# Optimization experiments

Hardware: AMD Instinct MI355X
Metric: run time of the kernel (lower is better)

## Reference

```python
import jax, jax.numpy as jnp
import numpy as np

B, T, N, CIN = 16, 34, 1000, 32
DC, OC, E, DIL = 32, 64, 16000, 2


def _dilated_conv(xt, w, b, d):
    # xt: [B, C, N, T], w: [O, C, 1, 2] -> [B, O, N, T-d]
    Tt = xt.shape[-1]
    y = (jnp.einsum('bcnt,oc->bont', xt[..., :Tt - d], w[:, :, 0, 0])
         + jnp.einsum('bcnt,oc->bont', xt[..., d:], w[:, :, 0, 1]))
    return y + b[None, :, None, None]


def setup_inputs() -> dict:
    key = jax.random.key(0)
    ks = jax.random.split(key, 12)
    return {
        'x': jax.random.normal(ks[0], (B, T, N, CIN), jnp.float32),
        'edge_index': jax.random.randint(ks[1], (2, E), 0, N, jnp.int32),
        'edge_weight': jax.random.uniform(ks[2], (E,), jnp.float32),
        'w_gate1': jax.random.normal(ks[3], (DC, CIN, 1, 2), jnp.float32) * 0.1,
        'b_gate1': jax.random.normal(ks[4], (DC,), jnp.float32) * 0.1,
        'w_gate2': jax.random.normal(ks[5], (DC, CIN, 1, 2), jnp.float32) * 0.1,
        'b_gate2': jax.random.normal(ks[6], (DC,), jnp.float32) * 0.1,
        'w_gcn': jax.random.normal(ks[7], (CIN, DC), jnp.float32) * 0.1,
        'b_gcn': jax.random.normal(ks[8], (CIN,), jnp.float32) * 0.1,
        'w_out': jax.random.normal(ks[9], (OC, CIN, 1, 1), jnp.float32) * 0.1,
        'b_out': jax.random.normal(ks[10], (OC,), jnp.float32) * 0.1,
    }


def reference(x, edge_index, edge_weight, w_gate1, b_gate1, w_gate2, b_gate2,
              w_gcn, b_gcn, w_out, b_out):
    # [B,T,N,C] -> [B,C,N,T]  (torch transpose(-3,-1))
    xt = jnp.transpose(x, (0, 3, 2, 1))
    g1 = jnp.tanh(_dilated_conv(xt, w_gate1, b_gate1, DIL))
    g2 = jax.nn.sigmoid(_dilated_conv(xt, w_gate2, b_gate2, DIL))
    out1 = g1 * g2                      # [B, DC, N, T']
    Tp = out1.shape[-1]
    gated = jnp.transpose(out1, (0, 3, 2, 1))        # [B, T', N, DC]
    out2 = gated.reshape(B * Tp, N, DC)              # G graphs, shared adjacency

    # --- GCNConv (PyG defaults: add self-loops w=1, symmetric normalization) ---
    src, dst = edge_index[0], edge_index[1]
    loop = jnp.arange(N, dtype=edge_index.dtype)
    src_a = jnp.concatenate([src, loop])
    dst_a = jnp.concatenate([dst, loop])
    w_a = jnp.concatenate([edge_weight, jnp.ones((N,), edge_weight.dtype)])
    deg = jax.ops.segment_sum(w_a, dst_a, num_segments=N)
    dis = jnp.where(deg > 0, jax.lax.rsqrt(jnp.where(deg > 0, deg, 1.0)), 0.0)
    norm = dis[src_a] * w_a * dis[dst_a]
    # All G graphs share the adjacency -> build it once densely (N x N is tiny)
    A = jnp.zeros((N, N), out2.dtype).at[dst_a, src_a].add(norm)
    xw = jnp.einsum('gnd,cd->gnc', out2, w_gcn)      # linear: x @ W^T
    gcn = jnp.einsum('ij,gjc->gic', A, xw) + b_gcn   # propagate + bias
    gcn = gcn.reshape(B, Tp, N, CIN)
    # dropout: deterministic (eval) identity

    # 1x1 output conv (applied in NCHW, equivalent to per-channel linear)
    y = jnp.einsum('btnc,oc->btno', gcn, w_out[:, :, 0, 0]) + b_out
    return (out1, y)
```

## Files before the change

### kernel.cpp

```cpp
#include <hip/hip_runtime.h>
#include <math.h>

#define Bq 16
#define Tq 34
#define Nq 1000
#define Cq 32
#define OCq 64
#define Eq 16000
#define TPq 32
#define Gq (Bq*TPq)

typedef _Float16 f16;
typedef f16  f16x8 __attribute__((ext_vector_type(8)));
typedef float f32x4 __attribute__((ext_vector_type(4)));

__device__ __forceinline__ float fast_tanh(float x) {
    float xc = fminf(fmaxf(x, -15.f), 15.f);
    float u  = __expf(2.f * xc);
    return 1.f - 2.f * __builtin_amdgcn_rcpf(u + 1.f);
}
__device__ __forceinline__ float fast_sigmoid(float x) {
    float xc = fminf(fmaxf(x, -30.f), 30.f);
    return __builtin_amdgcn_rcpf(1.f + __expf(-xc));
}
__device__ __forceinline__ unsigned bf16_bits(float f) {
    unsigned u = __float_as_uint(f);
    return (u + 0x7fffu + ((u >> 16) & 1u)) >> 16;
}
__device__ __forceinline__ unsigned pack_bf16x2(float lo, float hi) {
    return bf16_bits(lo) | (bf16_bits(hi) << 16);
}

__global__ __launch_bounds__(640) void k_prep(
    const float* __restrict__ wg1, const float* __restrict__ wg2,
    const float* __restrict__ wgcn, f16* __restrict__ fragbuf)
{
    const int tid = threadIdx.x;
    if (tid < 512) {
        const int fid  = tid >> 6;
        const int lane = tid & 63;
        const int gate  = fid >> 2;
        const int otile = (fid >> 1) & 1;
        const int ks    = fid & 1;
        const float* w = gate ? wg2 : wg1;
        const int o = otile*16 + (lane & 15);
        f16* dst = fragbuf + (size_t)fid*512 + lane*8;
        #pragma unroll
        for (int j = 0; j < 8; j++) {
            const int c = (lane >> 4)*8 + j;
            dst[j] = (f16)w[o*64 + c*2 + ks];
        }
    } else if (tid < 640) {
        const int l2 = tid - 512;
        const int ctile = l2 >> 6;
        const int lane  = l2 & 63;
        const int c = ctile*16 + (lane & 15);
        f16* dst = fragbuf + (size_t)8*512 + ((size_t)ctile*64 + lane)*8;
        #pragma unroll
        for (int j = 0; j < 8; j++) {
            const int o = (lane >> 4)*8 + j;
            dst[j] = (f16)wgcn[c*32 + o];
        }
    }
}

__global__ __launch_bounds__(128) void k_conv(
    const float* __restrict__ x,
    const float* __restrict__ bg1, const float* __restrict__ bg2,
    const f16* __restrict__ fragbuf,
    float* __restrict__ out1, uint2* __restrict__ xw2)
{
    __shared__ f16 goS[32*40];
    const int tid  = threadIdx.x;
    const int w    = tid >> 6;
    const int lane = tid & 63;
    const int b    = blockIdx.x / Nq;
    const int n    = blockIdx.x % Nq;
    const int tq   = lane & 15;
    const int cg   = lane >> 4;

    const uint4* fb = (const uint4*)fragbuf;
    union cvu { uint4 u; f16x8 h; };
    cvu A1k0; A1k0.u = fb[(0 + w*2 + 0)*64 + lane];
    cvu A1k1; A1k1.u = fb[(0 + w*2 + 1)*64 + lane];
    cvu A2k0; A2k0.u = fb[(4 + w*2 + 0)*64 + lane];
    cvu A2k1; A2k1.u = fb[(4 + w*2 + 1)*64 + lane];

    f16x8 Bf[2][2];
    #pragma unroll
    for (int tt = 0; tt < 2; tt++) {
        #pragma unroll
        for (int ks = 0; ks < 2; ks++) {
            const float* xp = x + (((size_t)(b*Tq + tt*16 + tq + ks*2))*Nq + n)*Cq + cg*8;
            const float4 lo = *(const float4*)xp;
            const float4 hi = *(const float4*)(xp + 4);
            f16x8 h;
            h[0]=(f16)lo.x; h[1]=(f16)lo.y; h[2]=(f16)lo.z; h[3]=(f16)lo.w;
            h[4]=(f16)hi.x; h[5]=(f16)hi.y; h[6]=(f16)hi.z; h[7]=(f16)hi.w;
            Bf[tt][ks] = h;
        }
    }

    f32x4 acc1[2] = {{0.f,0.f,0.f,0.f},{0.f,0.f,0.f,0.f}};
    f32x4 acc2[2] = {{0.f,0.f,0.f,0.f},{0.f,0.f,0.f,0.f}};
    #pragma unroll
    for (int tt = 0; tt < 2; tt++) {
        acc1[tt] = __builtin_amdgcn_mfma_f32_16x16x32_f16(A1k0.h, Bf[tt][0], acc1[tt], 0,0,0);
        acc1[tt] = __builtin_amdgcn_mfma_f32_16x16x32_f16(A1k1.h, Bf[tt][1], acc1[tt], 0,0,0);
        acc2[tt] = __builtin_amdgcn_mfma_f32_16x16x32_f16(A2k0.h, Bf[tt][0], acc2[tt], 0,0,0);
        acc2[tt] = __builtin_amdgcn_mfma_f32_16x16x32_f16(A2k1.h, Bf[tt][1], acc2[tt], 0,0,0);
    }

    const int obase = w*16 + cg*4;
    const float4 b1 = *(const float4*)&bg1[obase];
    const float4 b2 = *(const float4*)&bg2[obase];
    const float b1a[4] = {b1.x,b1.y,b1.z,b1.w};
    const float b2a[4] = {b2.x,b2.y,b2.z,b2.w};

    float* o1base = out1 + ((size_t)b*Cq + obase)*(Nq*TPq) + (size_t)n*TPq;
    #pragma unroll
    for (int tt = 0; tt < 2; tt++) {
        const int t = tt*16 + tq;
        f16* gp = &goS[t*40 + obase];
        #pragma unroll
        for (int r = 0; r < 4; r++) {
            const float a1 = acc1[tt][r] + b1a[r];
            const float a2 = acc2[tt][r] + b2a[r];
            const float go = fast_tanh(a1) * fast_sigmoid(a2);
            o1base[(size_t)r*(Nq*TPq) + t] = go;
            gp[r] = (f16)go;
        }
    }
    __syncthreads();

    cvu A2f; A2f.u = fb[8*64 + w*64 + lane];
    #pragma unroll
    for (int tt = 0; tt < 2; tt++) {
        const int t = tt*16 + tq;
        const f16x8 B2 = *(const f16x8*)&goS[t*40 + cg*8];
        f32x4 xa = {0.f,0.f,0.f,0.f};
        xa = __builtin_amdgcn_mfma_f32_16x16x32_f16(A2f.h, B2, xa, 0,0,0);
        const int g  = b*32 + t;
        const int s  = g >> 8;
        const int gl = g & 255;
        const int cbase = w*16 + cg*4;
        uint2 u;
        u.x = pack_bf16x2(xa[0], xa[1]);
        u.y = pack_bf16x2(xa[2], xa[3]);
        xw2[((size_t)(n*2 + s)*8 + (cbase >> 2))*256 + gl] = u;
    }
}

__global__ __launch_bounds__(1024) void k_graph(
    const int* __restrict__ ei, const float* __restrict__ ew,
    float* __restrict__ dis_g, int* __restrict__ rowstart_g,
    int* __restrict__ col, float* __restrict__ val)
{
    __shared__ float deg[Nq];
    __shared__ int   cnt[Nq];
    __shared__ int   pos[Nq];
    __shared__ float diss[Nq];
    __shared__ int   ssum[1024];
    const int tid = threadIdx.x;

    for (int n = tid; n < Nq; n += 1024) { deg[n] = 1.0f; cnt[n] = 0; }
    __syncthreads();
    for (int e = tid; e < Eq; e += 1024) {
        int d = ei[Eq + e];
        atomicAdd(&deg[d], ew[e]);
        atomicAdd(&cnt[d], 1);
    }
    __syncthreads();
    const int v = (tid < Nq) ? cnt[tid] : 0;
    ssum[tid] = v;
    __syncthreads();
    for (int off = 1; off < 1024; off <<= 1) {
        int add = (tid >= off) ? ssum[tid - off] : 0;
        __syncthreads();
        ssum[tid] += add;
        __syncthreads();
    }
    if (tid < Nq) {
        int excl = ssum[tid] - v;
        pos[tid] = excl;
        rowstart_g[tid] = excl;
        float di = rsqrtf(deg[tid]);
        diss[tid] = di;
        dis_g[tid] = di;
        if (tid == Nq-1) rowstart_g[Nq] = ssum[tid];
    }
    __syncthreads();
    for (int e = tid; e < Eq; e += 1024) {
        int srce = ei[e], d = ei[Eq + e];
        int slot = atomicAdd(&pos[d], 1);
        col[slot] = srce;
        val[slot] = diss[srce] * ew[e] * diss[d];
    }
}

__global__ __launch_bounds__(256) void k_gcn(
    const uint2* __restrict__ xw2, const int* __restrict__ rowstart,
    const int* __restrict__ colv, const float* __restrict__ valv,
    const float* __restrict__ dis, const float* __restrict__ bgcn,
    const float* __restrict__ wout, const float* __restrict__ bout,
    float* __restrict__ y)
{
    __shared__ float woT[Cq*OCq];
    __shared__ int   scol[64];
    __shared__ float sval[64];
    const int tid = threadIdx.x;
    const int s   = blockIdx.x / Nq;
    const int i   = blockIdx.x - s*Nq;

    for (int k = tid; k < Cq*OCq; k += 256) {
        int o = k & 63, c = k >> 6;
        woT[k] = wout[o*Cq + c];
    }

    float acc[Cq];
    #pragma unroll
    for (int c = 0; c < Cq; c++) acc[c] = 0.f;

    const int r0 = rowstart[i], r1 = rowstart[i+1];
    const int total = r1 - r0 + 1;
    const float dii = dis[i];

    for (int base = 0; base < total; base += 64) {
        const int cnt = min(64, total - base);
        __syncthreads();
        if (tid < cnt) {
            int k = base + tid;
            if (k == 0) { scol[tid] = i; sval[tid] = dii*dii; }
            else        { scol[tid] = colv[r0 + k - 1]; sval[tid] = valv[r0 + k - 1]; }
        }
        __syncthreads();
        for (int k = 0; k < cnt; k++) {
            const int   sc = scol[k];
            const float sv = sval[k];
            const uint2* rp = xw2 + ((size_t)(sc*2 + s)*8)*256 + tid;
            uint2 v[8];
            #pragma unroll
            for (int cg = 0; cg < 8; cg++) v[cg] = rp[cg*256];
            #pragma unroll
            for (int cg = 0; cg < 8; cg++) {
                acc[4*cg+0] = fmaf(sv, __uint_as_float(v[cg].x << 16),          acc[4*cg+0]);
                acc[4*cg+1] = fmaf(sv, __uint_as_float(v[cg].x & 0xffff0000u), acc[4*cg+1]);
                acc[4*cg+2] = fmaf(sv, __uint_as_float(v[cg].y << 16),          acc[4*cg+2]);
                acc[4*cg+3] = fmaf(sv, __uint_as_float(v[cg].y & 0xffff0000u), acc[4*cg+3]);
            }
        }
    }

    #pragma unroll
    for (int c4 = 0; c4 < 8; c4++) {
        const float4 bg = *(const float4*)&bgcn[4*c4];
        acc[4*c4+0] += bg.x; acc[4*c4+1] += bg.y;
        acc[4*c4+2] += bg.z; acc[4*c4+3] += bg.w;
    }

    const int g = s*256 + tid;
    float* yp = y + ((size_t)g*Nq + i)*OCq;
    #pragma unroll
    for (int h = 0; h < 2; h++) {
        float yr[32];
        #pragma unroll
        for (int q = 0; q < 32; q++) yr[q] = bout[h*32 + q];
        #pragma unroll
        for (int c = 0; c < Cq; c++) {
            const float ga = acc[c];
            const float* wrow = &woT[c*OCq + h*32];
            #pragma unroll
            for (int q4 = 0; q4 < 8; q4++) {
                const float4 w = *(const float4*)&wrow[4*q4];
                yr[4*q4+0] = fmaf(ga, w.x, yr[4*q4+0]);
                yr[4*q4+1] = fmaf(ga, w.y, yr[4*q4+1]);
                yr[4*q4+2] = fmaf(ga, w.z, yr[4*q4+2]);
                yr[4*q4+3] = fmaf(ga, w.w, yr[4*q4+3]);
            }
        }
        #pragma unroll
        for (int q4 = 0; q4 < 8; q4++) {
            float4 vv;
            vv.x = yr[4*q4+0]; vv.y = yr[4*q4+1];
            vv.z = yr[4*q4+2]; vv.w = yr[4*q4+3];
            *(float4*)&yp[h*32 + 4*q4] = vv;
        }
    }
}

extern "C" void kernel_launch(void* const* d_in, const int* in_sizes, int n_in,
                              void* d_out, int out_size, void* d_ws, size_t ws_size,
                              hipStream_t stream)
{
    const float* x    = (const float*)d_in[0];
    const int*   ei   = (const int*)  d_in[1];
    const float* ew   = (const float*)d_in[2];
    const float* wg1  = (const float*)d_in[3];
    const float* bg1  = (const float*)d_in[4];
    const float* wg2  = (const float*)d_in[5];
    const float* bg2  = (const float*)d_in[6];
    const float* wgcn = (const float*)d_in[7];
    const float* bgcn = (const float*)d_in[8];
    const float* wout = (const float*)d_in[9];
    const float* bout = (const float*)d_in[10];

    float* out1 = (float*)d_out;
    float* y    = out1 + (size_t)Bq*Cq*Nq*TPq;

    char* ws = (char*)d_ws;
    uint2* xwt = (uint2*)ws; ws += sizeof(unsigned short)*(size_t)Nq*Gq*Cq;
    float* dis = (float*)ws; ws += sizeof(float)*Nq;
    float* val = (float*)ws; ws += sizeof(float)*Eq;
    int*   col = (int*)ws;   ws += sizeof(int)*Eq;
    int*   rowstart = (int*)ws; ws += sizeof(int)*(Nq+4);
    f16*   fragbuf  = (f16*)ws; ws += sizeof(f16)*(10*512);

    k_prep<<<1, 640, 0, stream>>>(wg1, wg2, wgcn, fragbuf);
    k_conv<<<Bq*Nq, 128, 0, stream>>>(x, bg1, bg2, fragbuf, out1, xwt);
    k_graph<<<1, 1024, 0, stream>>>(ei, ew, dis, rowstart, col, val);
    k_gcn<<<2*Nq, 256, 0, stream>>>(xwt, rowstart, col, val, dis,
                                    bgcn, wout, bout, y);
}
```

Before: 490.3 us.

## Restructure GCN kernel: 64-thread blocks, uint4 loads, prefetch, nontemporal stores

Changes the xw intermediate layout so each thread loads 8 bf16 channels per uint4, and splits the GCN work into 8x more 64-thread blocks with a one-step software prefetch of the next neighbor row. The transposed output weight moves into k_prep and is read from global memory instead of being rebuilt in LDS by every block. Stores of out1 and y use nontemporal hints to reduce cache pollution. Risks include weight reads from global or L1 inside the inner FMA loop and a lower per-block thread count.

```diff
diff --git a/kernel.cpp b/kernel.cpp
--- a/kernel.cpp
+++ b/kernel.cpp
@@ -31,9 +31,10 @@
     return bf16_bits(lo) | (bf16_bits(hi) << 16);
 }
 
-__global__ __launch_bounds__(640) void k_prep(
+__global__ __launch_bounds__(1024) void k_prep(
     const float* __restrict__ wg1, const float* __restrict__ wg2,
-    const float* __restrict__ wgcn, f16* __restrict__ fragbuf)
+    const float* __restrict__ wgcn, const float* __restrict__ wout,
+    f16* __restrict__ fragbuf, float* __restrict__ woTg)
 {
     const int tid = threadIdx.x;
     if (tid < 512) {
@@ -62,6 +63,8 @@
             dst[j] = (f16)wgcn[c*32 + o];
         }
     }
+    for (int k = tid; k < Cq*OCq; k += 1024)
+        woTg[k] = wout[(k & 63)*Cq + (k >> 6)];
 }
 
 __global__ __launch_bounds__(128) void k_conv(
@@ -127,7 +130,7 @@
             const float a1 = acc1[tt][r] + b1a[r];
             const float a2 = acc2[tt][r] + b2a[r];
             const float go = fast_tanh(a1) * fast_sigmoid(a2);
-            o1base[(size_t)r*(Nq*TPq) + t] = go;
+            __builtin_nontemporal_store(go, &o1base[(size_t)r*(Nq*TPq) + t]);
             gp[r] = (f16)go;
         }
     }
@@ -147,7 +150,9 @@
         uint2 u;
         u.x = pack_bf16x2(xa[0], xa[1]);
         u.y = pack_bf16x2(xa[2], xa[3]);
-        xw2[((size_t)(n*2 + s)*8 + (cbase >> 2))*256 + gl] = u;
+        const int c8   = cbase >> 3;
+        const int half = (cbase >> 2) & 1;
+        xw2[(((size_t)(n*2 + s)*4 + c8)*256 + gl)*2 + half] = u;
     }
 }
 
@@ -198,24 +203,31 @@
     }
 }
 
-__global__ __launch_bounds__(256) void k_gcn(
-    const uint2* __restrict__ xw2, const int* __restrict__ rowstart,
+#define ACC8(vv, c8) do { \
+    acc[8*(c8)+0] = fmaf(sv, __uint_as_float((vv).x << 16),          acc[8*(c8)+0]); \
+    acc[8*(c8)+1] = fmaf(sv, __uint_as_float((vv).x & 0xffff0000u), acc[8*(c8)+1]); \
+    acc[8*(c8)+2] = fmaf(sv, __uint_as_float((vv).y << 16),          acc[8*(c8)+2]); \
+    acc[8*(c8)+3] = fmaf(sv, __uint_as_float((vv).y & 0xffff0000u), acc[8*(c8)+3]); \
+    acc[8*(c8)+4] = fmaf(sv, __uint_as_float((vv).z << 16),          acc[8*(c8)+4]); \
+    acc[8*(c8)+5] = fmaf(sv, __uint_as_float((vv).z & 0xffff0000u), acc[8*(c8)+5]); \
+    acc[8*(c8)+6] = fmaf(sv, __uint_as_float((vv).w << 16),          acc[8*(c8)+6]); \
+    acc[8*(c8)+7] = fmaf(sv, __uint_as_float((vv).w & 0xffff0000u), acc[8*(c8)+7]); \
+} while (0)
+
+__global__ __launch_bounds__(64) void k_gcn(
+    const uint4* __restrict__ xw4, const int* __restrict__ rowstart,
     const int* __restrict__ colv, const float* __restrict__ valv,
     const float* __restrict__ dis, const float* __restrict__ bgcn,
-    const float* __restrict__ wout, const float* __restrict__ bout,
+    const float* __restrict__ woTg, const float* __restrict__ bout,
     float* __restrict__ y)
 {
-    __shared__ float woT[Cq*OCq];
     __shared__ int   scol[64];
     __shared__ float sval[64];
-    const int tid = threadIdx.x;
-    const int s   = blockIdx.x / Nq;
-    const int i   = blockIdx.x - s*Nq;
-
-    for (int k = tid; k < Cq*OCq; k += 256) {
-        int o = k & 63, c = k >> 6;
-        woT[k] = wout[o*Cq + c];
-    }
+    const int tid  = threadIdx.x;
+    const int pair = blockIdx.x & 7;
+    const int i    = blockIdx.x >> 3;
+    const int s    = pair & 1;
+    const int gl   = (pair >> 1)*64 + tid;
 
     float acc[Cq];
     #pragma unroll
@@ -224,6 +236,7 @@
     const int r0 = rowstart[i], r1 = rowstart[i+1];
     const int total = r1 - r0 + 1;
     const float dii = dis[i];
+    const uint4* xg = xw4 + (size_t)s*1024 + gl;
 
     for (int base = 0; base < total; base += 64) {
         const int cnt = min(64, total - base);
@@ -234,21 +247,18 @@
             else        { scol[tid] = colv[r0 + k - 1]; sval[tid] = valv[r0 + k - 1]; }
         }
         __syncthreads();
-        for (int k = 0; k < cnt; k++) {
-            const int   sc = scol[k];
-            const float sv = sval[k];
-            const uint2* rp = xw2 + ((size_t)(sc*2 + s)*8)*256 + tid;
-            uint2 v[8];
-            #pragma unroll
-            for (int cg = 0; cg < 8; cg++) v[cg] = rp[cg*256];
-            #pragma unroll
-            for (int cg = 0; cg < 8; cg++) {
-                acc[4*cg+0] = fmaf(sv, __uint_as_float(v[cg].x << 16),          acc[4*cg+0]);
-                acc[4*cg+1] = fmaf(sv, __uint_as_float(v[cg].x & 0xffff0000u), acc[4*cg+1]);
-                acc[4*cg+2] = fmaf(sv, __uint_as_float(v[cg].y << 16),          acc[4*cg+2]);
-                acc[4*cg+3] = fmaf(sv, __uint_as_float(v[cg].y & 0xffff0000u), acc[4*cg+3]);
-            }
-        }
+
+        const uint4* rp = xg + (size_t)scol[0]*2048;
+        float sv = sval[0];
+        uint4 va0 = rp[0], va1 = rp[256], va2 = rp[512], va3 = rp[768];
+        for (int k = 1; k < cnt; k++) {
+            const uint4* rq = xg + (size_t)scol[k]*2048;
+            const float svn = sval[k];
+            const uint4 vb0 = rq[0], vb1 = rq[256], vb2 = rq[512], vb3 = rq[768];
+            ACC8(va0, 0); ACC8(va1, 1); ACC8(va2, 2); ACC8(va3, 3);
+            va0 = vb0; va1 = vb1; va2 = vb2; va3 = vb3; sv = svn;
+        }
+        ACC8(va0, 0); ACC8(va1, 1); ACC8(va2, 2); ACC8(va3, 3);
     }
 
     #pragma unroll
@@ -258,7 +268,7 @@
         acc[4*c4+2] += bg.z; acc[4*c4+3] += bg.w;
     }
 
-    const int g = s*256 + tid;
+    const int g = s*256 + gl;
     float* yp = y + ((size_t)g*Nq + i)*OCq;
     #pragma unroll
     for (int h = 0; h < 2; h++) {
@@ -268,7 +278,7 @@
         #pragma unroll
         for (int c = 0; c < Cq; c++) {
             const float ga = acc[c];
-            const float* wrow = &woT[c*OCq + h*32];
+            const float* wrow = &woTg[c*OCq + h*32];
             #pragma unroll
             for (int q4 = 0; q4 < 8; q4++) {
                 const float4 w = *(const float4*)&wrow[4*q4];
@@ -280,10 +290,10 @@
         }
         #pragma unroll
         for (int q4 = 0; q4 < 8; q4++) {
-            float4 vv;
-            vv.x = yr[4*q4+0]; vv.y = yr[4*q4+1];
-            vv.z = yr[4*q4+2]; vv.w = yr[4*q4+3];
-            *(float4*)&yp[h*32 + 4*q4] = vv;
+            f32x4 vv;
+            vv[0] = yr[4*q4+0]; vv[1] = yr[4*q4+1];
+            vv[2] = yr[4*q4+2]; vv[3] = yr[4*q4+3];
+            __builtin_nontemporal_store(vv, (f32x4*)&yp[h*32 + 4*q4]);
         }
     }
 }
@@ -314,10 +324,11 @@
     int*   col = (int*)ws;   ws += sizeof(int)*Eq;
     int*   rowstart = (int*)ws; ws += sizeof(int)*(Nq+4);
     f16*   fragbuf  = (f16*)ws; ws += sizeof(f16)*(10*512);
-
-    k_prep<<<1, 640, 0, stream>>>(wg1, wg2, wgcn, fragbuf);
+    float* woTg     = (float*)ws; ws += sizeof(float)*Cq*OCq;
+
+    k_prep<<<1, 1024, 0, stream>>>(wg1, wg2, wgcn, wout, fragbuf, woTg);
     k_conv<<<Bq*Nq, 128, 0, stream>>>(x, bg1, bg2, fragbuf, out1, xwt);
     k_graph<<<1, 1024, 0, stream>>>(ei, ew, dis, rowstart, col, val);
-    k_gcn<<<2*Nq, 256, 0, stream>>>(xwt, rowstart, col, val, dis,
-                                    bgcn, wout, bout, y);
-}
+    k_gcn<<<8*Nq, 64, 0, stream>>>((const uint4*)xwt, rowstart, col, val, dis,
+                                   bgcn, woTg, bout, y);
+}
```

After: 706.9 us. 44.2% more time.
